# Kernel optimization log

Measured on AMD Instinct MI355X. Metric: run time of the kernel, lower is better.

## Reference

```python
import jax, jax.numpy as jnp
import numpy as np
from jax import lax

N_TAPS = 27  # 3x3x3 kernel

def _gather_one(xb, ti, hi, wi):
    # xb: (C,T,H,W); ti/hi/wi: (T,H,W) int32. Zero-fill outside bounds.
    C, T, H, W = xb.shape
    valid = (ti >= 0) & (ti < T) & (hi >= 0) & (hi < H) & (wi >= 0) & (wi < W)
    lin = (jnp.clip(ti, 0, T - 1) * H + jnp.clip(hi, 0, H - 1)) * W + jnp.clip(wi, 0, W - 1)
    v = jnp.take(xb.reshape(C, -1), lin.reshape(-1), axis=1).reshape(C, T, H, W)
    return v * valid.astype(xb.dtype)

_gather = jax.vmap(_gather_one)  # over batch

def _trilinear(x, t, h, w):
    # x: (B,C,T,H,W); t/h/w: (B,T,H,W) float sample coordinates.
    t0, h0, w0 = jnp.floor(t), jnp.floor(h), jnp.floor(w)
    lt, lh, lw = t - t0, h - h0, w - w0
    t0i, h0i, w0i = t0.astype(jnp.int32), h0.astype(jnp.int32), w0.astype(jnp.int32)
    acc = 0.0
    for ti, wt in ((t0i, 1.0 - lt), (t0i + 1, lt)):
        for hi, wh in ((h0i, 1.0 - lh), (h0i + 1, lh)):
            for wi, ww in ((w0i, 1.0 - lw), (w0i + 1, lw)):
                acc = acc + _gather(x, ti, hi, wi) * (wt * wh * ww)[:, None]
    return acc  # (B,C,T,H,W)

def _deform_conv3d(x, offset_w, offset_b, weight):
    # x: (B,Cin,T,H,W). Offset layout: (B, 3, 27, T, H, W), axis1=(dt,dh,dw),
    # tap index k = kt*9 + kh*3 + kw. stride=1, padding=1, dilation=1, no bias.
    off = lax.conv_general_dilated(
        x, offset_w, (1, 1, 1), [(1, 1)] * 3,
        dimension_numbers=("NCDHW", "OIDHW", "NCDHW"))
    off = off + offset_b[None, :, None, None, None]
    B, _, T, H, W = off.shape
    off = off.reshape(B, 3, N_TAPS, T, H, W)
    tg = jnp.arange(T, dtype=x.dtype)[:, None, None]
    hg = jnp.arange(H, dtype=x.dtype)[None, :, None]
    wg = jnp.arange(W, dtype=x.dtype)[None, None, :]
    out = jnp.zeros((B, weight.shape[0], T, H, W), x.dtype)
    for k in range(N_TAPS):
        kt, kh, kw = k // 9, (k // 3) % 3, k % 3
        t = tg + (kt - 1) + off[:, 0, k]
        h = hg + (kh - 1) + off[:, 1, k]
        w = wg + (kw - 1) + off[:, 2, k]
        s = _trilinear(x, t, h, w)  # (B,Cin,T,H,W)
        out = out + jnp.einsum('bcthw,oc->bothw', s, weight[:, :, kt, kh, kw])
    return out

def setup_inputs() -> dict:
    key = jax.random.key(0)
    ks = jax.random.split(key, 4)
    B, T, C, H, W = 1, 4, 64, 128, 128
    x = jax.random.normal(ks[0], (B, T, C, H, W), jnp.float32)
    # small init scale keeps predicted offsets in a realistic +-2px range
    offset_w = jax.random.normal(ks[1], (3 * N_TAPS, C, 3, 3, 3), jnp.float32) * 0.02
    offset_b = jnp.zeros((3 * N_TAPS,), jnp.float32)
    weight = jax.random.normal(ks[2], (C, C, 3, 3, 3), jnp.float32) * 0.02
    gamma = jax.random.normal(ks[3], (1,), jnp.float32) * 0.1
    return {"x": x, "offset_w": offset_w, "offset_b": offset_b,
            "weight": weight, "gamma": gamma}

def reference(x, offset_w, offset_b, weight, gamma):
    xp = jnp.transpose(x, (0, 2, 1, 3, 4))  # (B,C,T,H,W)
    xc = _deform_conv3d(xp, offset_w, offset_b, weight)
    return gamma[0] * jnp.transpose(xc, (0, 2, 1, 3, 4)) + x
```

## Files before the change

### kernel.cpp

```cpp
#include <hip/hip_runtime.h>
#include <cmath>

#define Cc 64
#define Hh 128
#define Ww 128
#define HW_ 16384
#define THW_ 65536
#define CHW_ 1048576
#define NT 27

typedef unsigned short ushort_t;
typedef _Float16 f16x2 __attribute__((ext_vector_type(2)));
typedef _Float16 f16x8 __attribute__((ext_vector_type(8)));
typedef __fp16 fp16x2_alt __attribute__((ext_vector_type(2)));
typedef float floatx4 __attribute__((ext_vector_type(4)));

union U32H2 { unsigned u; f16x2 h; };

static __device__ inline ushort_t f2h(float f) {
  union { _Float16 h; ushort_t u; } v;
  v.h = (_Float16)f;
  return v.u;
}

static __device__ inline unsigned pk2(float a) {
  union { fp16x2_alt h; unsigned u; } v;
  v.h = __builtin_amdgcn_cvt_pkrtz(a, a);
  return v.u;
}

#if defined(__has_builtin)
#if __has_builtin(__builtin_amdgcn_make_buffer_rsrc) && __has_builtin(__builtin_amdgcn_raw_buffer_load_b32)
#define USE_BUF 1
#endif
#endif
#ifndef USE_BUF
#define USE_BUF 0
#endif

struct XtBuf {
#if USE_BUF
  __amdgpu_buffer_rsrc_t r;
#else
  const unsigned* p;
#endif
};

static __device__ inline XtBuf mkbuf(const ushort_t* xt) {
  XtBuf b;
#if USE_BUF
  b.r = __builtin_amdgcn_make_buffer_rsrc((void*)xt, (short)0, 8388608, 0x00020000);
#else
  b.p = (const unsigned*)xt;
#endif
  return b;
}

static __device__ inline unsigned xload(const XtBuf& b, unsigned voff) {
#if USE_BUF
  return (unsigned)__builtin_amdgcn_raw_buffer_load_b32(b.r, (int)voff, 0, 0);
#else
  return b.p[voff >> 2];
#endif
}


__global__ __launch_bounds__(256) void prep(
    const float* __restrict__ offset_w,
    const float* __restrict__ weight,
    ushort_t* __restrict__ w2frag,
    ushort_t* __restrict__ wfrag)
{
  int e = blockIdx.x * 256 + threadIdx.x;
  if (e < 165888) {
    int j = e & 7, ln = (e >> 3) & 63, kh2 = (e >> 9) & 1, r = e >> 10;
    int ot = r % 6, k = r / 6;
    int oc = ot * 16 + (ln & 15);
    int c  = kh2 * 32 + (ln >> 4) * 8 + j;
    float v = (oc < 81) ? offset_w[(oc * 64 + c) * 27 + k] : 0.f;
    w2frag[e] = f2h(v);
  }
  if (e < 110592) {
    int j = e & 7, ln = (e >> 3) & 63, kh2 = (e >> 9) & 1, r = e >> 10;
    int ot = r & 3, k = r >> 2;
    int o = ot * 16 + (ln & 15);
    int c = kh2 * 32 + (ln >> 4) * 8 + j;
    wfrag[e] = f2h(weight[(o * 64 + c) * 27 + k]);
  }
}

__global__ __launch_bounds__(256) void transpose_x(
    const float* __restrict__ x, ushort_t* __restrict__ xt)
{
  __shared__ float tile[64][65];
  int b = blockIdx.x;
  int wblk = b & 1;
  int th = b >> 1;
  int h = th & 127;
  int t = th >> 7;
  int w0 = wblk * 64;
  int lane = threadIdx.x & 63;
  int quad = threadIdx.x >> 6;
  #pragma unroll
  for (int cc = 0; cc < 16; ++cc) {
    int c = cc * 4 + quad;
    tile[c][lane] = x[t * CHW_ + c * HW_ + h * Ww + w0 + lane];
  }
  __syncthreads();
  #pragma unroll
  for (int ww = 0; ww < 16; ++ww) {
    int w = ww * 4 + quad;
    xt[(size_t)(t * HW_ + h * Ww + w0 + w) * 64 + lane] = f2h(tile[lane][w]);
  }
}

__global__ __launch_bounds__(256, 4) void offconv(
    const ushort_t* __restrict__ xt,
    const ushort_t* __restrict__ w2frag,
    const float* __restrict__ ob,
    float* __restrict__ off)
{
  __shared__ __align__(16) char lds[24960];
  ushort_t* S = (ushort_t*)lds;
  float* Dbuf = (float*)lds;
  int lane = threadIdx.x & 63;
  int wavei = __builtin_amdgcn_readfirstlane(threadIdx.x >> 6);
  int quad = lane >> 4;
  int m16 = lane & 15;
  int hlf = lane >> 5;
  int lo4 = (lane & 31) * 4;
  int p0 = blockIdx.x * 64;
  int t = p0 >> 14;
  int h = (p0 >> 7) & 127;
  int w0 = p0 & 127;
  XtBuf xb = mkbuf(xt);

  floatx4 acc[6];
  #pragma unroll
  for (int i = 0; i < 6; ++i) acc[i] = (floatx4){0.f, 0.f, 0.f, 0.f};

  unsigned pd[8];

  auto issue = [&](int k) {
    int kt = k / 9, kh = (k / 3) % 3, kw = k % 3;
    int ts = t + kt - 1, hs = h + kh - 1;
    int tsc = min(max(ts, 0), 3);
    int hsc = min(max(hs, 0), 127);
    int sbase = tsc * HW_ + hsc * Ww;
    #pragma unroll
    for (int j = 0; j < 8; ++j) {
      int prow = wavei * 16 + j * 2 + hlf;
      int wc = w0 + prow + kw - 1;
      int wcc = min(max(wc, 0), 127);
      pd[j] = xload(xb, ((unsigned)(sbase + wcc) << 7) + lo4);
    }
  };

  issue(0);
  #pragma unroll 1
  for (int k = 0; k < NT; ++k) {
    int kt = k / 9, kh = (k / 3) % 3, kw = k % 3;
    int ts = t + kt - 1, hs = h + kh - 1;
    bool rowok = ((unsigned)ts < 4u) && ((unsigned)hs < 128u);
    #pragma unroll
    for (int j = 0; j < 8; ++j) {
      int prow = wavei * 16 + j * 2 + hlf;
      int wc = w0 + prow + kw - 1;
      bool ok = rowok && ((unsigned)wc < 128u);
      *(unsigned*)((char*)S + prow * 144 + lo4) = ok ? pd[j] : 0u;
    }
    issue(k + 1 < NT ? k + 1 : NT - 1);
    const ushort_t* srow = S + (wavei * 16 + m16) * 72 + quad * 8;
    f16x8 af0 = *(const f16x8*)srow;
    f16x8 af1 = *(const f16x8*)(srow + 32);
    #pragma unroll
    for (int ot = 0; ot < 6; ++ot) {
      const ushort_t* wb = w2frag + (size_t)((k * 6 + ot) * 2) * 512 + lane * 8;
      f16x8 b0 = *(const f16x8*)(wb);
      f16x8 b1 = *(const f16x8*)(wb + 512);
      acc[ot] = __builtin_amdgcn_mfma_f32_16x16x32_f16(af0, b0, acc[ot], 0, 0, 0);
      acc[ot] = __builtin_amdgcn_mfma_f32_16x16x32_f16(af1, b1, acc[ot], 0, 0, 0);
    }
  }
  __syncthreads();
  #pragma unroll
  for (int ot = 0; ot < 6; ++ot)
    #pragma unroll
    for (int r = 0; r < 4; ++r)
      Dbuf[(ot * 16 + m16) * 65 + wavei * 16 + quad * 4 + r] = acc[ot][r];
  __syncthreads();
  for (int i = threadIdx.x; i < 81 * 64; i += 256) {
    int oc = i >> 6, p = i & 63;
    off[(size_t)oc * THW_ + p0 + p] = Dbuf[oc * 65 + p] + ob[oc];
  }
}

__global__ __launch_bounds__(256, 4) void deform(
    const float* __restrict__ x,
    const ushort_t* __restrict__ xt,
    const float* __restrict__ off,
    const ushort_t* __restrict__ wfrag,
    const float* __restrict__ gamma,
    float* __restrict__ out)
{
  __shared__ __align__(16) char lds[16640];
  ushort_t* S = (ushort_t*)lds;
  unsigned* msite = (unsigned*)(lds + 9216);
  unsigned* mwt   = (unsigned*)(lds + 11264);
  float* Dbuf = (float*)lds;
  int lane = threadIdx.x & 63;
  int wavei = __builtin_amdgcn_readfirstlane(threadIdx.x >> 6);
  int quad = lane >> 4;
  int m16 = lane & 15;
  int hlf = lane >> 5;
  int lo4 = (lane & 31) * 4;
  int p0 = blockIdx.x * 64;
  int t = p0 >> 14;
  int h = (p0 >> 7) & 127;
  int w0 = p0 & 127;
  XtBuf xb = mkbuf(xt);

  floatx4 acc[4];
  #pragma unroll
  for (int i = 0; i < 4; ++i) acc[i] = (floatx4){0.f, 0.f, 0.f, 0.f};

  int pl = wavei * 16 + m16;
  int pm = p0 + pl;
  int aq = quad >> 1, bq = quad & 1;
  const float* offT = off + pm;

  float dt_c = offT[(size_t)(0 * NT + 0) * THW_];
  float dh_c = offT[(size_t)(1 * NT + 0) * THW_];
  float dw_c = offT[(size_t)(2 * NT + 0) * THW_];

  #pragma unroll 1
  for (int k = 0; k < NT; ++k) {
    int kn = (k + 1 < NT) ? k + 1 : NT - 1;
    float dt_n = offT[(size_t)(0 * NT + kn) * THW_];
    float dh_n = offT[(size_t)(1 * NT + kn) * THW_];
    float dw_n = offT[(size_t)(2 * NT + kn) * THW_];

    int kt = k / 9, kh = (k / 3) % 3, kw = k % 3;
    float tf = (float)(t + kt - 1) + dt_c;
    float hf = (float)(h + kh - 1) + dh_c;
    float wf = (float)(w0 + pl + kw - 1) + dw_c;
    float tF = floorf(tf), hF = floorf(hf), wF = floorf(wf);
    float lt = tf - tF, lh_ = hf - hF, lw_ = wf - wF;
    int t0 = (int)tF, h0 = (int)hF, wq_ = (int)wF;
    int ti = t0 + aq;
    float wt_ = (aq ? lt : 1.f - lt) * (((unsigned)ti < 4u) ? 1.f : 0.f);
    int tic = min(max(ti, 0), 3);
    int hi = h0 + bq;
    float wh_ = (bq ? lh_ : 1.f - lh_) * (((unsigned)hi < 128u) ? 1.f : 0.f);
    int hic = min(max(hi, 0), 127);
    int base2 = tic * HW_ + hic * Ww;
    float bw = wt_ * wh_;
    int wi0 = wq_;
    float ww0 = (1.f - lw_) * (((unsigned)wi0 < 128u) ? 1.f : 0.f);
    int wi0c = min(max(wi0, 0), 127);
    int wi1 = wq_ + 1;
    float ww1 = lw_ * (((unsigned)wi1 < 128u) ? 1.f : 0.f);
    int wi1c = min(max(wi1, 0), 127);
    uint2 sp_;
    sp_.x = (unsigned)(base2 + wi0c) << 7;
    sp_.y = (unsigned)(base2 + wi1c) << 7;
    *(uint2*)&msite[pl * 8 + quad * 2] = sp_;
    uint2 wp_;
    wp_.x = pk2(bw * ww0);
    wp_.y = pk2(bw * ww1);
    *(uint2*)&mwt[pl * 8 + quad * 2] = wp_;

    unsigned dreg[8][8];
    #pragma unroll
    for (int j = 0; j < 8; ++j) {
      int prow = wavei * 16 + j * 2 + hlf;
      const uint4* spp = (const uint4*)&msite[prow * 8];
      uint4 s03 = spp[0], s47 = spp[1];
      dreg[j][0] = xload(xb, s03.x + lo4);
      dreg[j][1] = xload(xb, s03.y + lo4);
      dreg[j][2] = xload(xb, s03.z + lo4);
      dreg[j][3] = xload(xb, s03.w + lo4);
      dreg[j][4] = xload(xb, s47.x + lo4);
      dreg[j][5] = xload(xb, s47.y + lo4);
      dreg[j][6] = xload(xb, s47.z + lo4);
      dreg[j][7] = xload(xb, s47.w + lo4);
    }
    #pragma unroll
    for (int j = 0; j < 8; ++j) {
      int prow = wavei * 16 + j * 2 + hlf;
      const uint4* wpp = (const uint4*)&mwt[prow * 8];
      uint4 w03 = wpp[0], w47 = wpp[1];
      U32H2 z; z.u = 0;
      f16x2 a2l = z.h, a2h = z.h;
      U32H2 du, wu;
      du.u = dreg[j][0]; wu.u = w03.x; a2l += wu.h * du.h;
      du.u = dreg[j][1]; wu.u = w03.y; a2h += wu.h * du.h;
      du.u = dreg[j][2]; wu.u = w03.z; a2l += wu.h * du.h;
      du.u = dreg[j][3]; wu.u = w03.w; a2h += wu.h * du.h;
      du.u = dreg[j][4]; wu.u = w47.x; a2l += wu.h * du.h;
      du.u = dreg[j][5]; wu.u = w47.y; a2h += wu.h * du.h;
      du.u = dreg[j][6]; wu.u = w47.z; a2l += wu.h * du.h;
      du.u = dreg[j][7]; wu.u = w47.w; a2h += wu.h * du.h;
      U32H2 res;
      res.h = a2l + a2h;
      *(unsigned*)((char*)S + prow * 144 + lo4) = res.u;
    }
    const ushort_t* srow = S + (wavei * 16 + m16) * 72 + quad * 8;
    f16x8 af0 = *(const f16x8*)srow;
    f16x8 af1 = *(const f16x8*)(srow + 32);
    #pragma unroll
    for (int ot = 0; ot < 4; ++ot) {
      const ushort_t* wb = wfrag + (size_t)((k * 4 + ot) * 2) * 512 + lane * 8;
      f16x8 b0 = *(const f16x8*)(wb);
      f16x8 b1 = *(const f16x8*)(wb + 512);
      acc[ot] = __builtin_amdgcn_mfma_f32_16x16x32_f16(af0, b0, acc[ot], 0, 0, 0);
      acc[ot] = __builtin_amdgcn_mfma_f32_16x16x32_f16(af1, b1, acc[ot], 0, 0, 0);
    }
    dt_c = dt_n; dh_c = dh_n; dw_c = dw_n;
  }
  __syncthreads();
  #pragma unroll
  for (int ot = 0; ot < 4; ++ot)
    #pragma unroll
    for (int r = 0; r < 4; ++r)
      Dbuf[(ot * 16 + m16) * 65 + wavei * 16 + quad * 4 + r] = acc[ot][r];
  __syncthreads();
  float g = gamma[0];
  for (int i = threadIdx.x; i < 64 * 64; i += 256) {
    int oc = i >> 6, p = i & 63;
    size_t oi = (size_t)t * CHW_ + (size_t)oc * HW_ + (size_t)h * Ww + w0 + p;
    out[oi] = fmaf(g, Dbuf[oc * 65 + p], x[oi]);
  }
}

extern "C" void kernel_launch(void* const* d_in, const int* in_sizes, int n_in,
                              void* d_out, int out_size, void* d_ws, size_t ws_size,
                              hipStream_t stream) {
  (void)in_sizes; (void)n_in; (void)out_size; (void)ws_size;
  const float* x        = (const float*)d_in[0];
  const float* offset_w = (const float*)d_in[1];
  const float* offset_b = (const float*)d_in[2];
  const float* weight   = (const float*)d_in[3];
  const float* gamma    = (const float*)d_in[4];
  float* out = (float*)d_out;
  float* wsf = (float*)d_ws;
  float*    off    = wsf;
  ushort_t* xt     = (ushort_t*)(wsf + 5308416);
  ushort_t* wfrag  = (ushort_t*)(wsf + 7405568);
  ushort_t* w2frag = (ushort_t*)(wsf + 7460864);

  hipLaunchKernelGGL(prep, dim3(648), dim3(256), 0, stream,
                     offset_w, weight, w2frag, wfrag);
  hipLaunchKernelGGL(transpose_x, dim3(1024), dim3(256), 0, stream, x, xt);
  hipLaunchKernelGGL(offconv, dim3(1024), dim3(256), 0, stream,
                     xt, w2frag, offset_b, off);
  hipLaunchKernelGGL(deform, dim3(1024), dim3(256), 0, stream,
                     x, xt, off, wfrag, gamma, out);
}
```

Measured before the change: 228.7 us.

## Widen gather loads to 128-bit and swizzle block order for locality

Both the offset-conv and deform kernels now load 16 bytes per lane (8 channels) with buffer_load_b128 instead of 4 bytes, so each lane handles 8 channels of one pixel row rather than 2 channels across many rows. This cuts the number of load instructions per sample by a factor of four. The block-to-pixel mapping is also permuted so concurrently running blocks are spread across t/h rows, which may change cache reuse. The deform kernel's occupancy hint drops from 4 to 3 waves-per-EU to leave room for the larger register footprint of 16 in-flight 128-bit loads, which could reduce latency hiding.

```diff
diff --git a/kernel.cpp b/kernel.cpp
--- a/kernel.cpp
+++ b/kernel.cpp
@@ -14,6 +14,7 @@
 typedef _Float16 f16x8 __attribute__((ext_vector_type(8)));
 typedef __fp16 fp16x2_alt __attribute__((ext_vector_type(2)));
 typedef float floatx4 __attribute__((ext_vector_type(4)));
+typedef unsigned uint4v __attribute__((ext_vector_type(4)));
 
 union U32H2 { unsigned u; f16x2 h; };
 
@@ -30,7 +31,7 @@
 }
 
 #if defined(__has_builtin)
-#if __has_builtin(__builtin_amdgcn_make_buffer_rsrc) && __has_builtin(__builtin_amdgcn_raw_buffer_load_b32)
+#if __has_builtin(__builtin_amdgcn_make_buffer_rsrc) && __has_builtin(__builtin_amdgcn_raw_buffer_load_b32) && __has_builtin(__builtin_amdgcn_raw_buffer_load_b128)
 #define USE_BUF 1
 #endif
 #endif
@@ -42,7 +43,7 @@
 #if USE_BUF
   __amdgpu_buffer_rsrc_t r;
 #else
-  const unsigned* p;
+  const char* p;
 #endif
 };
 
@@ -51,16 +52,16 @@
 #if USE_BUF
   b.r = __builtin_amdgcn_make_buffer_rsrc((void*)xt, (short)0, 8388608, 0x00020000);
 #else
-  b.p = (const unsigned*)xt;
+  b.p = (const char*)xt;
 #endif
   return b;
 }
 
-static __device__ inline unsigned xload(const XtBuf& b, unsigned voff) {
+static __device__ inline uint4v xload4(const XtBuf& b, unsigned voff) {
 #if USE_BUF
-  return (unsigned)__builtin_amdgcn_raw_buffer_load_b32(b.r, (int)voff, 0, 0);
+  return __builtin_amdgcn_raw_buffer_load_b128(b.r, (int)voff, 0, 0);
 #else
-  return b.p[voff >> 2];
+  return *(const uint4v*)(b.p + voff);
 #endif
 }
 
@@ -127,9 +128,10 @@
   int wavei = __builtin_amdgcn_readfirstlane(threadIdx.x >> 6);
   int quad = lane >> 4;
   int m16 = lane & 15;
-  int hlf = lane >> 5;
-  int lo4 = (lane & 31) * 4;
-  int p0 = blockIdx.x * 64;
+  int g8 = lane >> 3;
+  unsigned coff = (unsigned)((lane & 7) * 16);
+  int bid0 = blockIdx.x;
+  int p0 = ((bid0 & 7) * 128 + (bid0 >> 3)) * 64;
   int t = p0 >> 14;
   int h = (p0 >> 7) & 127;
   int w0 = p0 & 127;
@@ -139,7 +141,7 @@
   #pragma unroll
   for (int i = 0; i < 6; ++i) acc[i] = (floatx4){0.f, 0.f, 0.f, 0.f};
 
-  unsigned pd[8];
+  uint4v pd[2];
 
   auto issue = [&](int k) {
     int kt = k / 9, kh = (k / 3) % 3, kw = k % 3;
@@ -148,11 +150,11 @@
     int hsc = min(max(hs, 0), 127);
     int sbase = tsc * HW_ + hsc * Ww;
     #pragma unroll
-    for (int j = 0; j < 8; ++j) {
-      int prow = wavei * 16 + j * 2 + hlf;
+    for (int b = 0; b < 2; ++b) {
+      int prow = wavei * 16 + b * 8 + g8;
       int wc = w0 + prow + kw - 1;
       int wcc = min(max(wc, 0), 127);
-      pd[j] = xload(xb, ((unsigned)(sbase + wcc) << 7) + lo4);
+      pd[b] = xload4(xb, ((unsigned)(sbase + wcc) << 7) + coff);
     }
   };
 
@@ -163,11 +165,13 @@
     int ts = t + kt - 1, hs = h + kh - 1;
     bool rowok = ((unsigned)ts < 4u) && ((unsigned)hs < 128u);
     #pragma unroll
-    for (int j = 0; j < 8; ++j) {
-      int prow = wavei * 16 + j * 2 + hlf;
+    for (int b = 0; b < 2; ++b) {
+      int prow = wavei * 16 + b * 8 + g8;
       int wc = w0 + prow + kw - 1;
       bool ok = rowok && ((unsigned)wc < 128u);
-      *(unsigned*)((char*)S + prow * 144 + lo4) = ok ? pd[j] : 0u;
+      uint4v v = pd[b];
+      if (!ok) v = (uint4v){0u, 0u, 0u, 0u};
+      *(uint4v*)((char*)S + prow * 144 + coff) = v;
     }
     issue(k + 1 < NT ? k + 1 : NT - 1);
     const ushort_t* srow = S + (wavei * 16 + m16) * 72 + quad * 8;
@@ -195,7 +199,12 @@
   }
 }
 
-__global__ __launch_bounds__(256, 4) void deform(
+#define SITE(W, D, A0, A1, A2, A3) \
+  { U32H2 wu; wu.u = (W); U32H2 q0, q1, q2, q3; \
+    q0.u = (D)[0]; q1.u = (D)[1]; q2.u = (D)[2]; q3.u = (D)[3]; \
+    A0 += wu.h * q0.h; A1 += wu.h * q1.h; A2 += wu.h * q2.h; A3 += wu.h * q3.h; }
+
+__global__ __launch_bounds__(256, 3) void deform(
     const float* __restrict__ x,
     const ushort_t* __restrict__ xt,
     const float* __restrict__ off,
@@ -212,9 +221,10 @@
   int wavei = __builtin_amdgcn_readfirstlane(threadIdx.x >> 6);
   int quad = lane >> 4;
   int m16 = lane & 15;
-  int hlf = lane >> 5;
-  int lo4 = (lane & 31) * 4;
-  int p0 = blockIdx.x * 64;
+  int g8 = lane >> 3;
+  unsigned coff = (unsigned)((lane & 7) * 16);
+  int bid0 = blockIdx.x;
+  int p0 = ((bid0 & 7) * 128 + (bid0 >> 3)) * 64;
   int t = p0 >> 14;
   int h = (p0 >> 7) & 127;
   int w0 = p0 & 127;
@@ -227,6 +237,8 @@
   int pl = wavei * 16 + m16;
   int pm = p0 + pl;
   int aq = quad >> 1, bq = quad & 1;
+  int rowA = wavei * 16 + g8;
+  int rowB = rowA + 8;
   const float* offT = off + pm;
 
   float dt_c = offT[(size_t)(0 * NT + 0) * THW_];
@@ -270,41 +282,66 @@
     wp_.y = pk2(bw * ww1);
     *(uint2*)&mwt[pl * 8 + quad * 2] = wp_;
 
-    unsigned dreg[8][8];
-    #pragma unroll
-    for (int j = 0; j < 8; ++j) {
-      int prow = wavei * 16 + j * 2 + hlf;
-      const uint4* spp = (const uint4*)&msite[prow * 8];
-      uint4 s03 = spp[0], s47 = spp[1];
-      dreg[j][0] = xload(xb, s03.x + lo4);
-      dreg[j][1] = xload(xb, s03.y + lo4);
-      dreg[j][2] = xload(xb, s03.z + lo4);
-      dreg[j][3] = xload(xb, s03.w + lo4);
-      dreg[j][4] = xload(xb, s47.x + lo4);
-      dreg[j][5] = xload(xb, s47.y + lo4);
-      dreg[j][6] = xload(xb, s47.z + lo4);
-      dreg[j][7] = xload(xb, s47.w + lo4);
-    }
-    #pragma unroll
-    for (int j = 0; j < 8; ++j) {
-      int prow = wavei * 16 + j * 2 + hlf;
-      const uint4* wpp = (const uint4*)&mwt[prow * 8];
-      uint4 w03 = wpp[0], w47 = wpp[1];
+    const uint4* spA = (const uint4*)&msite[rowA * 8];
+    uint4 sA0 = spA[0], sA1 = spA[1];
+    const uint4* spB = (const uint4*)&msite[rowB * 8];
+    uint4 sB0 = spB[0], sB1 = spB[1];
+    uint4v stA0 = xload4(xb, sA0.x + coff);
+    uint4v stA1 = xload4(xb, sA0.y + coff);
+    uint4v stA2 = xload4(xb, sA0.z + coff);
+    uint4v stA3 = xload4(xb, sA0.w + coff);
+    uint4v stA4 = xload4(xb, sA1.x + coff);
+    uint4v stA5 = xload4(xb, sA1.y + coff);
+    uint4v stA6 = xload4(xb, sA1.z + coff);
+    uint4v stA7 = xload4(xb, sA1.w + coff);
+    uint4v stB0 = xload4(xb, sB0.x + coff);
+    uint4v stB1 = xload4(xb, sB0.y + coff);
+    uint4v stB2 = xload4(xb, sB0.z + coff);
+    uint4v stB3 = xload4(xb, sB0.w + coff);
+    uint4v stB4 = xload4(xb, sB1.x + coff);
+    uint4v stB5 = xload4(xb, sB1.y + coff);
+    uint4v stB6 = xload4(xb, sB1.z + coff);
+    uint4v stB7 = xload4(xb, sB1.w + coff);
+
+    {
+      const uint4* wpA = (const uint4*)&mwt[rowA * 8];
+      uint4 w03 = wpA[0], w47 = wpA[1];
       U32H2 z; z.u = 0;
-      f16x2 a2l = z.h, a2h = z.h;
-      U32H2 du, wu;
-      du.u = dreg[j][0]; wu.u = w03.x; a2l += wu.h * du.h;
-      du.u = dreg[j][1]; wu.u = w03.y; a2h += wu.h * du.h;
-      du.u = dreg[j][2]; wu.u = w03.z; a2l += wu.h * du.h;
-      du.u = dreg[j][3]; wu.u = w03.w; a2h += wu.h * du.h;
-      du.u = dreg[j][4]; wu.u = w47.x; a2l += wu.h * du.h;
-      du.u = dreg[j][5]; wu.u = w47.y; a2h += wu.h * du.h;
-      du.u = dreg[j][6]; wu.u = w47.z; a2l += wu.h * du.h;
-      du.u = dreg[j][7]; wu.u = w47.w; a2h += wu.h * du.h;
-      U32H2 res;
-      res.h = a2l + a2h;
-      *(unsigned*)((char*)S + prow * 144 + lo4) = res.u;
-    }
+      f16x2 e0 = z.h, e1 = z.h, e2 = z.h, e3 = z.h;
+      f16x2 o0 = z.h, o1 = z.h, o2 = z.h, o3 = z.h;
+      SITE(w03.x, stA0, e0, e1, e2, e3)
+      SITE(w03.y, stA1, o0, o1, o2, o3)
+      SITE(w03.z, stA2, e0, e1, e2, e3)
+      SITE(w03.w, stA3, o0, o1, o2, o3)
+      SITE(w47.x, stA4, e0, e1, e2, e3)
+      SITE(w47.y, stA5, o0, o1, o2, o3)
+      SITE(w47.z, stA6, e0, e1, e2, e3)
+      SITE(w47.w, stA7, o0, o1, o2, o3)
+      U32H2 r0, r1, r2, r3;
+      r0.h = e0 + o0; r1.h = e1 + o1; r2.h = e2 + o2; r3.h = e3 + o3;
+      uint4v res = {r0.u, r1.u, r2.u, r3.u};
+      *(uint4v*)((char*)S + rowA * 144 + coff) = res;
+    }
+    {
+      const uint4* wpB = (const uint4*)&mwt[rowB * 8];
+      uint4 w03 = wpB[0], w47 = wpB[1];
+      U32H2 z; z.u = 0;
+      f16x2 e0 = z.h, e1 = z.h, e2 = z.h, e3 = z.h;
+      f16x2 o0 = z.h, o1 = z.h, o2 = z.h, o3 = z.h;
+      SITE(w03.x, stB0, e0, e1, e2, e3)
+      SITE(w03.y, stB1, o0, o1, o2, o3)
+      SITE(w03.z, stB2, e0, e1, e2, e3)
+      SITE(w03.w, stB3, o0, o1, o2, o3)
+      SITE(w47.x, stB4, e0, e1, e2, e3)
+      SITE(w47.y, stB5, o0, o1, o2, o3)
+      SITE(w47.z, stB6, e0, e1, e2, e3)
+      SITE(w47.w, stB7, o0, o1, o2, o3)
+      U32H2 r0, r1, r2, r3;
+      r0.h = e0 + o0; r1.h = e1 + o1; r2.h = e2 + o2; r3.h = e3 + o3;
+      uint4v res = {r0.u, r1.u, r2.u, r3.u};
+      *(uint4v*)((char*)S + rowB * 144 + coff) = res;
+    }
+
     const ushort_t* srow = S + (wavei * 16 + m16) * 72 + quad * 8;
     f16x8 af0 = *(const f16x8*)srow;
     f16x8 af1 = *(const f16x8*)(srow + 32);
```

After: 283.1 us. +23.8%, slower.
